# Performance work log

Hardware: AMD Instinct MI355X
Metric: run time of the kernel (lower is better)

The kernel has to match this reference:

```python
import jax, jax.numpy as jnp
import numpy as np

B, C, H, W = 4, 512, 64, 64
CK = C // 8  # key/query channels


def setup_inputs() -> dict:
    key = jax.random.key(0)
    ks = jax.random.split(key, 4)
    x = jax.random.normal(ks[0], (B, C, H, W), dtype=jnp.float32)
    # 1x1 conv weights -> plain [out, in] matrices; fan-in scaled like torch default-ish
    Wf = jax.random.normal(ks[1], (CK, C), dtype=jnp.float32) * (1.0 / np.sqrt(C))
    Wg = jax.random.normal(ks[2], (CK, C), dtype=jnp.float32) * (1.0 / np.sqrt(C))
    Wh = jax.random.normal(ks[3], (C, C), dtype=jnp.float32) * (1.0 / np.sqrt(C))
    bf = jnp.zeros((CK,), dtype=jnp.float32)
    bg = jnp.zeros((CK,), dtype=jnp.float32)
    bh = jnp.zeros((C,), dtype=jnp.float32)
    gamma = jnp.zeros((1,), dtype=jnp.float32)
    return {"x": x, "Wf": Wf, "bf": bf, "Wg": Wg, "bg": bg, "Wh": Wh, "bh": bh, "gamma": gamma}


def reference(x, Wf, bf, Wg, bg, Wh, bh, gamma):
    b, c, h, w = x.shape
    n = h * w
    xf = x.reshape(b, c, n)  # [B, C, N]
    # 1x1 convs == per-pixel linear maps
    f = jnp.einsum('kc,bcn->bkn', Wf, xf) + bf[None, :, None]  # [B, CK, N]
    g = jnp.einsum('kc,bcn->bkn', Wg, xf) + bg[None, :, None]  # [B, CK, N]
    hx = jnp.einsum('oc,bcn->bon', Wh, xf) + bh[None, :, None]  # [B, C, N]
    # energy[b,i,j] = sum_k f[b,k,i] * g[b,k,j]  (f_x.permute(0,2,1) @ g_x)
    energy = jnp.einsum('bki,bkj->bij', f, g)  # [B, N, N]
    attention = jax.nn.softmax(energy, axis=-1)
    # out[b,c,i] = sum_j hx[b,c,j] * attention[b,i,j]  (h_x @ attention^T)
    out = jnp.einsum('bcj,bij->bci', hx, attention)  # [B, C, N]
    out = out.reshape(b, c, h, w)
    return gamma[0] * out + x
```

## Files before the change

### kernel.cpp

```cpp
#include <hip/hip_runtime.h>
#include <hip/hip_bf16.h>

#define NB 4
#define CC 512
#define NN 4096
#define CKK 64

typedef _Float16 f16x4 __attribute__((ext_vector_type(4)));
typedef _Float16 f16x8 __attribute__((ext_vector_type(8)));
typedef float    f32x4 __attribute__((ext_vector_type(4)));

__device__ __forceinline__ void g2l16(const _Float16* g, _Float16* l) {
    __builtin_amdgcn_global_load_lds(
        (const __attribute__((address_space(1))) void*)g,
        (__attribute__((address_space(3))) void*)l, 16, 0, 0);
}

__device__ __forceinline__ void stage_tile(const _Float16* __restrict__ g, int ldg,
                                           _Float16* lds, int lane, int wave) {
    #pragma unroll
    for (int r = 0; r < 2; r++) {
        int q = r * 4 + wave;
        int row = q * 16 + (lane >> 2);
        int col = (lane & 3) * 8;
        g2l16(g + (size_t)row * ldg + col, lds + q * 512 + lane * 8);
    }
}

__launch_bounds__(256)
__global__ void convert_w(const float* __restrict__ Wf, const float* __restrict__ bf_,
                          const float* __restrict__ Wg, const float* __restrict__ bg_,
                          const float* __restrict__ Wh, const float* __restrict__ bh_,
                          _Float16* __restrict__ Wall, float* __restrict__ Ball) {
    int o = blockIdx.x;
    int t = threadIdx.x;
    const float* src;
    if (o < 64)       src = Wf + (size_t)o * CC;
    else if (o < 128) src = Wg + (size_t)(o - 64) * CC;
    else              src = Wh + (size_t)(o - 128) * CC;
    Wall[(size_t)o * CC + t]       = (_Float16)src[t];
    Wall[(size_t)o * CC + 256 + t] = (_Float16)src[256 + t];
    if (t == 0)
        Ball[o] = (o < 64) ? bf_[o] : (o < 128 ? bg_[o - 64] : bh_[o - 128]);
}

__launch_bounds__(256)
__global__ void proj_mfma(const float* __restrict__ x, const _Float16* __restrict__ Wall,
                          const float* __restrict__ Ball,
                          _Float16* __restrict__ Ft, _Float16* __restrict__ Gt,
                          _Float16* __restrict__ Hx) {
    const int N = NN, C = CC;
    int n0 = blockIdx.x * 128;
    int o0 = blockIdx.y * 128;
    int b  = blockIdx.z;
    const float* xb = x + (size_t)b * C * N;
    __shared__ _Float16 As[128 * 32];
    __shared__ _Float16 Bs[32 * 128];
    int tid = threadIdx.x, lane = tid & 63, wave = tid >> 6;
    int wm = wave & 1, wn = wave >> 1, lrow = lane & 15, quad = lane >> 4;
    int bk = tid >> 3;
    int bs = tid & 7;
    f32x4 acc[4][4] = {};
    for (int kc = 0; kc < C; kc += 32) {
        __syncthreads();
        stage_tile(Wall + (size_t)o0 * C + kc, C, As, lane, wave);
        const float* xr = xb + (size_t)(kc + bk) * N + n0 + bs * 16;
        float4 v0 = *(const float4*)(xr);
        float4 v1 = *(const float4*)(xr + 4);
        float4 v2 = *(const float4*)(xr + 8);
        float4 v3 = *(const float4*)(xr + 12);
        f16x8 h0 = { (_Float16)v0.x, (_Float16)v0.y, (_Float16)v0.z, (_Float16)v0.w,
                     (_Float16)v1.x, (_Float16)v1.y, (_Float16)v1.z, (_Float16)v1.w };
        f16x8 h1 = { (_Float16)v2.x, (_Float16)v2.y, (_Float16)v2.z, (_Float16)v2.w,
                     (_Float16)v3.x, (_Float16)v3.y, (_Float16)v3.z, (_Float16)v3.w };
        *(f16x8*)(Bs + bk * 128 + bs * 16)     = h0;
        *(f16x8*)(Bs + bk * 128 + bs * 16 + 8) = h1;
        __syncthreads();
        f16x8 af[4], bfr[4];
        #pragma unroll
        for (int mi = 0; mi < 4; mi++)
            af[mi] = *(const f16x8*)(As + (wm * 64 + mi * 16 + lrow) * 32 + quad * 8);
        #pragma unroll
        for (int ni = 0; ni < 4; ni++) {
            int n = wn * 64 + ni * 16 + lrow;
            #pragma unroll
            for (int j = 0; j < 8; j++)
                bfr[ni][j] = Bs[(quad * 8 + j) * 128 + n];
        }
        #pragma unroll
        for (int mi = 0; mi < 4; mi++)
            #pragma unroll
            for (int ni = 0; ni < 4; ni++)
                acc[mi][ni] = __builtin_amdgcn_mfma_f32_16x16x32_f16(af[mi], bfr[ni], acc[mi][ni], 0, 0, 0);
    }
    float bias_r[4][4];
    #pragma unroll
    for (int mi = 0; mi < 4; mi++)
        #pragma unroll
        for (int r = 0; r < 4; r++)
            bias_r[mi][r] = Ball[o0 + wm * 64 + mi * 16 + quad * 4 + r];
    _Float16* Ftb = Ft + (size_t)b * NN * CKK;
    _Float16* Gtb = Gt + (size_t)b * NN * CKK;
    _Float16* Hxb = Hx + (size_t)b * CC * N;
    #pragma unroll
    for (int mi = 0; mi < 4; mi++)
        #pragma unroll
        for (int ni = 0; ni < 4; ni++)
            #pragma unroll
            for (int r = 0; r < 4; r++) {
                int o = o0 + wm * 64 + mi * 16 + quad * 4 + r;
                int n = n0 + wn * 64 + ni * 16 + lrow;
                _Float16 v = (_Float16)(acc[mi][ni][r] + bias_r[mi][r]);
                if (o < 64)       Ftb[(size_t)n * CKK + o] = v;
                else if (o < 128) Gtb[(size_t)n * CKK + (o - 64)] = v;
                else              Hxb[(size_t)(o - 128) * N + n] = v;
            }
}

__launch_bounds__(256)
__global__ void energy_mfma(const _Float16* __restrict__ Ft, const _Float16* __restrict__ Gt,
                            _Float16* __restrict__ E, int r0, int Rstr) {
    const int N = NN;
    int b = blockIdx.z;
    const _Float16* Arow = Ft + (size_t)b * N * CKK + (size_t)(r0 + blockIdx.y * 128) * CKK;
    const _Float16* Brow = Gt + (size_t)b * N * CKK + (size_t)(blockIdx.x * 128) * CKK;
    _Float16* Eb = E + (size_t)b * Rstr * N + (size_t)blockIdx.y * 128 * N + blockIdx.x * 128;
    __shared__ _Float16 As[128 * 32];
    __shared__ _Float16 Bs[128 * 32];
    int tid = threadIdx.x, lane = tid & 63, wave = tid >> 6;
    int wm = wave & 1, wn = wave >> 1, lrow = lane & 15, quad = lane >> 4;
    f32x4 acc[4][4] = {};
    #pragma unroll
    for (int kc = 0; kc < CKK; kc += 32) {
        __syncthreads();
        stage_tile(Arow + kc, CKK, As, lane, wave);
        stage_tile(Brow + kc, CKK, Bs, lane, wave);
        __syncthreads();
        f16x8 af[4], bf[4];
        #pragma unroll
        for (int mi = 0; mi < 4; mi++)
            af[mi] = *(const f16x8*)(As + (wm * 64 + mi * 16 + lrow) * 32 + quad * 8);
        #pragma unroll
        for (int ni = 0; ni < 4; ni++)
            bf[ni] = *(const f16x8*)(Bs + (wn * 64 + ni * 16 + lrow) * 32 + quad * 8);
        #pragma unroll
        for (int mi = 0; mi < 4; mi++)
            #pragma unroll
            for (int ni = 0; ni < 4; ni++)
                acc[mi][ni] = __builtin_amdgcn_mfma_f32_16x16x32_f16(af[mi], bf[ni], acc[mi][ni], 0, 0, 0);
    }
    #pragma unroll
    for (int mi = 0; mi < 4; mi++)
        #pragma unroll
        for (int ni = 0; ni < 4; ni++)
            #pragma unroll
            for (int r = 0; r < 4; r++) {
                int il = wm * 64 + mi * 16 + quad * 4 + r;
                int j  = wn * 64 + ni * 16 + lrow;
                Eb[(size_t)il * N + j] = (_Float16)acc[mi][ni][r];
            }
}

__launch_bounds__(256)
__global__ void softmax_f16(_Float16* __restrict__ E, size_t bstride) {
    _Float16* p = E + blockIdx.y * bstride + (size_t)blockIdx.x * NN;
    int tid = threadIdx.x;
    f16x8 v0 = *(const f16x8*)(p + tid * 8);
    f16x8 v1 = *(const f16x8*)(p + 2048 + tid * 8);
    float f[16];
    #pragma unroll
    for (int j = 0; j < 8; j++) { f[j] = (float)v0[j]; f[8 + j] = (float)v1[j]; }
    float m = -1e30f;
    #pragma unroll
    for (int j = 0; j < 16; j++) m = fmaxf(m, f[j]);
    #pragma unroll
    for (int off = 32; off > 0; off >>= 1) m = fmaxf(m, __shfl_down(m, off));
    __shared__ float red[8];
    int wave = tid >> 6, lane = tid & 63;
    if (lane == 0) red[wave] = m;
    __syncthreads();
    m = fmaxf(fmaxf(red[0], red[1]), fmaxf(red[2], red[3]));
    float s = 0.f;
    #pragma unroll
    for (int j = 0; j < 16; j++) { f[j] = __expf(f[j] - m); s += f[j]; }
    #pragma unroll
    for (int off = 32; off > 0; off >>= 1) s += __shfl_down(s, off);
    if (lane == 0) red[4 + wave] = s;
    __syncthreads();
    s = red[4] + red[5] + red[6] + red[7];
    float inv = 1.0f / s;
    #pragma unroll
    for (int j = 0; j < 8; j++) { v0[j] = (_Float16)(f[j] * inv); v1[j] = (_Float16)(f[8 + j] * inv); }
    *(f16x8*)(p + tid * 8) = v0;
    *(f16x8*)(p + 2048 + tid * 8) = v1;
}

__launch_bounds__(256)
__global__ void out_mfma(const _Float16* __restrict__ Hx, const _Float16* __restrict__ P,
                         const float* __restrict__ x, const float* __restrict__ gamma,
                         float* __restrict__ out, int r0, int Rstr) {
    const int N = NN, C = CC;
    int b = blockIdx.z;
    int i0l = blockIdx.x * 128;
    int c0  = blockIdx.y * 128;
    const _Float16* Arow = Hx + (size_t)b * C * N + (size_t)c0 * N;
    const _Float16* Brow = P  + (size_t)b * Rstr * N + (size_t)i0l * N;
    __shared__ _Float16 As[128 * 32];
    __shared__ _Float16 Bs[128 * 32];
    int tid = threadIdx.x, lane = tid & 63, wave = tid >> 6;
    int wm = wave & 1, wn = wave >> 1, lrow = lane & 15, quad = lane >> 4;
    f32x4 acc[4][4] = {};
    for (int kc = 0; kc < N; kc += 32) {
        __syncthreads();
        stage_tile(Arow + kc, N, As, lane, wave);
        stage_tile(Brow + kc, N, Bs, lane, wave);
        __syncthreads();
        f16x8 af[4], bf[4];
        #pragma unroll
        for (int mi = 0; mi < 4; mi++)
            af[mi] = *(const f16x8*)(As + (wm * 64 + mi * 16 + lrow) * 32 + quad * 8);
        #pragma unroll
        for (int ni = 0; ni < 4; ni++)
            bf[ni] = *(const f16x8*)(Bs + (wn * 64 + ni * 16 + lrow) * 32 + quad * 8);
        #pragma unroll
        for (int mi = 0; mi < 4; mi++)
            #pragma unroll
            for (int ni = 0; ni < 4; ni++)
                acc[mi][ni] = __builtin_amdgcn_mfma_f32_16x16x32_f16(af[mi], bf[ni], acc[mi][ni], 0, 0, 0);
    }
    float gv = gamma[0];
    const float* xb = x + (size_t)b * C * N;
    float* ob = out + (size_t)b * C * N;
    int ig0 = r0 + i0l;
    #pragma unroll
    for (int mi = 0; mi < 4; mi++)
        #pragma unroll
        for (int ni = 0; ni < 4; ni++)
            #pragma unroll
            for (int r = 0; r < 4; r++) {
                int c = c0 + wm * 64 + mi * 16 + quad * 4 + r;
                int i = ig0 + wn * 64 + ni * 16 + lrow;
                ob[(size_t)c * N + i] = gv * acc[mi][ni][r] + xb[(size_t)c * N + i];
            }
}

extern "C" void kernel_launch(void* const* d_in, const int* in_sizes, int n_in,
                              void* d_out, int out_size, void* d_ws, size_t ws_size,
                              hipStream_t stream) {
    const float* x     = (const float*)d_in[0];
    const float* Wf    = (const float*)d_in[1];
    const float* bf    = (const float*)d_in[2];
    const float* Wg    = (const float*)d_in[3];
    const float* bg    = (const float*)d_in[4];
    const float* Wh    = (const float*)d_in[5];
    const float* bh    = (const float*)d_in[6];
    const float* gamma = (const float*)d_in[7];
    float* out = (float*)d_out;

    const int B = NB, C = CC, N = NN;

    char* wsb = (char*)d_ws;
    _Float16* Wall = (_Float16*)wsb;
    float*    Ball = (float*)(wsb + ((size_t)768 << 10));
    _Float16* Ft = (_Float16*)(wsb + ((size_t)1 << 20));
    _Float16* Gt = (_Float16*)(wsb + ((size_t)3 << 20));
    _Float16* Hx = (_Float16*)(wsb + ((size_t)5 << 20));
    _Float16* E  = (_Float16*)(wsb + ((size_t)21 << 20));
    size_t base = (size_t)21 << 20;
    size_t avail = (ws_size > base) ? ws_size - base : 0;
    size_t bytesPer128 = (size_t)B * N * 2 * 128;
    int R = (int)(avail / bytesPer128) * 128;
    if (R > N) R = N;
    if (R < 128) R = 128;

    convert_w<<<dim3(640), dim3(256), 0, stream>>>(Wf, bf, Wg, bg, Wh, bh, Wall, Ball);
    proj_mfma<<<dim3(N / 128, 5, B), dim3(256), 0, stream>>>(x, Wall, Ball, Ft, Gt, Hx);

    for (int r0 = 0; r0 < N; r0 += R) {
        int rows = (R < N - r0) ? R : (N - r0);
        energy_mfma<<<dim3(N / 128, rows / 128, B), dim3(256), 0, stream>>>(Ft, Gt, E, r0, R);
        softmax_f16<<<dim3(rows, B), dim3(256), 0, stream>>>(E, (size_t)R * N);
        out_mfma<<<dim3(rows / 128, C / 128, B), dim3(256), 0, stream>>>(Hx, E, x, gamma, out, r0, R);
    }
}
```

Baseline: 288.8 us.

## Fuse softmax statistics into energy epilogue and apply exp in output GEMM

```diff
diff --git a/kernel.cpp b/kernel.cpp
--- a/kernel.cpp
+++ b/kernel.cpp
@@ -119,7 +119,8 @@
 
 __launch_bounds__(256)
 __global__ void energy_mfma(const _Float16* __restrict__ Ft, const _Float16* __restrict__ Gt,
-                            _Float16* __restrict__ E, int r0, int Rstr) {
+                            _Float16* __restrict__ E, float* __restrict__ Mpart,
+                            float* __restrict__ Lpart, int r0, int Rstr) {
     const int N = NN;
     int b = blockIdx.z;
     const _Float16* Arow = Ft + (size_t)b * N * CKK + (size_t)(r0 + blockIdx.y * 128) * CKK;
@@ -127,6 +128,7 @@
     _Float16* Eb = E + (size_t)b * Rstr * N + (size_t)blockIdx.y * 128 * N + blockIdx.x * 128;
     __shared__ _Float16 As[128 * 32];
     __shared__ _Float16 Bs[128 * 32];
+    __shared__ float Sred[640];
     int tid = threadIdx.x, lane = tid & 63, wave = tid >> 6;
     int wm = wave & 1, wn = wave >> 1, lrow = lane & 15, quad = lane >> 4;
     f32x4 acc[4][4] = {};
@@ -159,44 +161,87 @@
                 int j  = wn * 64 + ni * 16 + lrow;
                 Eb[(size_t)il * N + j] = (_Float16)acc[mi][ni][r];
             }
-}
-
-__launch_bounds__(256)
-__global__ void softmax_f16(_Float16* __restrict__ E, size_t bstride) {
-    _Float16* p = E + blockIdx.y * bstride + (size_t)blockIdx.x * NN;
-    int tid = threadIdx.x;
-    f16x8 v0 = *(const f16x8*)(p + tid * 8);
-    f16x8 v1 = *(const f16x8*)(p + 2048 + tid * 8);
-    float f[16];
-    #pragma unroll
-    for (int j = 0; j < 8; j++) { f[j] = (float)v0[j]; f[8 + j] = (float)v1[j]; }
+    float mloc[16];
+    #pragma unroll
+    for (int mi = 0; mi < 4; mi++)
+        #pragma unroll
+        for (int r = 0; r < 4; r++) {
+            float v = acc[mi][0][r];
+            #pragma unroll
+            for (int ni = 1; ni < 4; ni++) v = fmaxf(v, acc[mi][ni][r]);
+            mloc[mi * 4 + r] = v;
+        }
+    #pragma unroll
+    for (int off = 1; off < 16; off <<= 1)
+        #pragma unroll
+        for (int s = 0; s < 16; s++)
+            mloc[s] = fmaxf(mloc[s], __shfl_xor(mloc[s], off));
+    {
+        float v = mloc[0];
+        #pragma unroll
+        for (int s = 1; s < 16; s++) v = (lrow == s) ? mloc[s] : v;
+        int row = wm * 64 + (lrow >> 2) * 16 + quad * 4 + (lrow & 3);
+        Sred[wn * 128 + row] = v;
+    }
+    __syncthreads();
+    if (tid < 128) Sred[512 + tid] = fmaxf(Sred[tid], Sred[128 + tid]);
+    __syncthreads();
+    float lloc[16];
+    #pragma unroll
+    for (int mi = 0; mi < 4; mi++)
+        #pragma unroll
+        for (int r = 0; r < 4; r++) {
+            int row = wm * 64 + mi * 16 + quad * 4 + r;
+            float m = Sred[512 + row];
+            float s = 0.f;
+            #pragma unroll
+            for (int ni = 0; ni < 4; ni++)
+                s += __expf((float)(_Float16)acc[mi][ni][r] - m);
+            lloc[mi * 4 + r] = s;
+        }
+    #pragma unroll
+    for (int off = 1; off < 16; off <<= 1)
+        #pragma unroll
+        for (int s = 0; s < 16; s++)
+            lloc[s] += __shfl_xor(lloc[s], off);
+    {
+        float v = lloc[0];
+        #pragma unroll
+        for (int s = 1; s < 16; s++) v = (lrow == s) ? lloc[s] : v;
+        int row = wm * 64 + (lrow >> 2) * 16 + quad * 4 + (lrow & 3);
+        Sred[256 + wn * 128 + row] = v;
+    }
+    __syncthreads();
+    if (tid < 128) {
+        size_t sidx = ((size_t)b * 32 + blockIdx.x) * Rstr + blockIdx.y * 128 + tid;
+        Mpart[sidx] = Sred[512 + tid];
+        Lpart[sidx] = Sred[256 + tid] + Sred[256 + 128 + tid];
+    }
+}
+
+__launch_bounds__(256)
+__global__ void combine_stats(const float* __restrict__ Mpart, const float* __restrict__ Lpart,
+                              float* __restrict__ Mrow, float* __restrict__ Linv,
+                              int rows, int Rstr) {
+    int b = blockIdx.y;
+    int i = blockIdx.x * 256 + threadIdx.x;
+    if (i >= rows) return;
+    const float* mp = Mpart + (size_t)b * 32 * Rstr + i;
+    const float* lp = Lpart + (size_t)b * 32 * Rstr + i;
     float m = -1e30f;
     #pragma unroll
-    for (int j = 0; j < 16; j++) m = fmaxf(m, f[j]);
-    #pragma unroll
-    for (int off = 32; off > 0; off >>= 1) m = fmaxf(m, __shfl_down(m, off));
-    __shared__ float red[8];
-    int wave = tid >> 6, lane = tid & 63;
-    if (lane == 0) red[wave] = m;
-    __syncthreads();
-    m = fmaxf(fmaxf(red[0], red[1]), fmaxf(red[2], red[3]));
-    float s = 0.f;
-    #pragma unroll
-    for (int j = 0; j < 16; j++) { f[j] = __expf(f[j] - m); s += f[j]; }
-    #pragma unroll
-    for (int off = 32; off > 0; off >>= 1) s += __shfl_down(s, off);
-    if (lane == 0) red[4 + wave] = s;
-    __syncthreads();
-    s = red[4] + red[5] + red[6] + red[7];
-    float inv = 1.0f / s;
-    #pragma unroll
-    for (int j = 0; j < 8; j++) { v0[j] = (_Float16)(f[j] * inv); v1[j] = (_Float16)(f[8 + j] * inv); }
-    *(f16x8*)(p + tid * 8) = v0;
-    *(f16x8*)(p + 2048 + tid * 8) = v1;
+    for (int jt = 0; jt < 32; jt++) m = fmaxf(m, mp[(size_t)jt * Rstr]);
+    float l = 0.f;
+    #pragma unroll
+    for (int jt = 0; jt < 32; jt++)
+        l += lp[(size_t)jt * Rstr] * __expf(mp[(size_t)jt * Rstr] - m);
+    Mrow[(size_t)b * Rstr + i] = m;
+    Linv[(size_t)b * Rstr + i] = 1.0f / l;
 }
 
 __launch_bounds__(256)
 __global__ void out_mfma(const _Float16* __restrict__ Hx, const _Float16* __restrict__ P,
+                         const float* __restrict__ Mrow, const float* __restrict__ Linv,
                          const float* __restrict__ x, const float* __restrict__ gamma,
                          float* __restrict__ out, int r0, int Rstr) {
     const int N = NN, C = CC;
@@ -204,16 +249,28 @@
     int i0l = blockIdx.x * 128;
     int c0  = blockIdx.y * 128;
     const _Float16* Arow = Hx + (size_t)b * C * N + (size_t)c0 * N;
-    const _Float16* Brow = P  + (size_t)b * Rstr * N + (size_t)i0l * N;
     __shared__ _Float16 As[128 * 32];
     __shared__ _Float16 Bs[128 * 32];
     int tid = threadIdx.x, lane = tid & 63, wave = tid >> 6;
     int wm = wave & 1, wn = wave >> 1, lrow = lane & 15, quad = lane >> 4;
+    int rB = tid >> 1;
+    int cs = (tid & 1) * 16;
+    const _Float16* bsrc = P + (size_t)b * Rstr * N + (size_t)(i0l + rB) * N + cs;
+    float mrow = Mrow[(size_t)b * Rstr + i0l + rB];
     f32x4 acc[4][4] = {};
     for (int kc = 0; kc < N; kc += 32) {
         __syncthreads();
         stage_tile(Arow + kc, N, As, lane, wave);
-        stage_tile(Brow + kc, N, Bs, lane, wave);
+        f16x8 e0 = *(const f16x8*)(bsrc + kc);
+        f16x8 e1 = *(const f16x8*)(bsrc + kc + 8);
+        f16x8 p0, p1;
+        #pragma unroll
+        for (int j = 0; j < 8; j++) {
+            p0[j] = (_Float16)__expf((float)e0[j] - mrow);
+            p1[j] = (_Float16)__expf((float)e1[j] - mrow);
+        }
+        *(f16x8*)(Bs + rB * 32 + cs)     = p0;
+        *(f16x8*)(Bs + rB * 32 + cs + 8) = p1;
         __syncthreads();
         f16x8 af[4], bf[4];
         #pragma unroll
@@ -229,6 +286,10 @@
                 acc[mi][ni] = __builtin_amdgcn_mfma_f32_16x16x32_f16(af[mi], bf[ni], acc[mi][ni], 0, 0, 0);
     }
     float gv = gamma[0];
+    float linv[4];
+    #pragma unroll
+    for (int ni = 0; ni < 4; ni++)
+        linv[ni] = Linv[(size_t)b * Rstr + i0l + wn * 64 + ni * 16 + lrow];
     const float* xb = x + (size_t)b * C * N;
     float* ob = out + (size_t)b * C * N;
     int ig0 = r0 + i0l;
@@ -240,7 +301,7 @@
             for (int r = 0; r < 4; r++) {
                 int c = c0 + wm * 64 + mi * 16 + quad * 4 + r;
                 int i = ig0 + wn * 64 + ni * 16 + lrow;
-                ob[(size_t)c * N + i] = gv * acc[mi][ni][r] + xb[(size_t)c * N + i];
+                ob[(size_t)c * N + i] = gv * acc[mi][ni][r] * linv[ni] + xb[(size_t)c * N + i];
             }
 }
 
@@ -265,8 +326,12 @@
     _Float16* Ft = (_Float16*)(wsb + ((size_t)1 << 20));
     _Float16* Gt = (_Float16*)(wsb + ((size_t)3 << 20));
     _Float16* Hx = (_Float16*)(wsb + ((size_t)5 << 20));
-    _Float16* E  = (_Float16*)(wsb + ((size_t)21 << 20));
-    size_t base = (size_t)21 << 20;
+    float* Mpart = (float*)(wsb + ((size_t)21 << 20));
+    float* Lpart = (float*)(wsb + ((size_t)23 << 20));
+    float* Mrow  = (float*)(wsb + ((size_t)25 << 20));
+    float* Linv  = (float*)(wsb + ((size_t)25 << 20) + ((size_t)512 << 10));
+    _Float16* E  = (_Float16*)(wsb + ((size_t)26 << 20));
+    size_t base = (size_t)26 << 20;
     size_t avail = (ws_size > base) ? ws_size - base : 0;
     size_t bytesPer128 = (size_t)B * N * 2 * 128;
     int R = (int)(avail / bytesPer128) * 128;
@@ -278,8 +343,11 @@
 
     for (int r0 = 0; r0 < N; r0 += R) {
         int rows = (R < N - r0) ? R : (N - r0);
-        energy_mfma<<<dim3(N / 128, rows / 128, B), dim3(256), 0, stream>>>(Ft, Gt, E, r0, R);
-        softmax_f16<<<dim3(rows, B), dim3(256), 0, stream>>>(E, (size_t)R * N);
-        out_mfma<<<dim3(rows / 128, C / 128, B), dim3(256), 0, stream>>>(Hx, E, x, gamma, out, r0, R);
-    }
-}
+        energy_mfma<<<dim3(N / 128, rows / 128, B), dim3(256), 0, stream>>>(
+            Ft, Gt, E, Mpart, Lpart, r0, R);
+        combine_stats<<<dim3((rows + 255) / 256, B), dim3(256), 0, stream>>>(
+            Mpart, Lpart, Mrow, Linv, rows, R);
+        out_mfma<<<dim3(rows / 128, C / 128, B), dim3(256), 0, stream>>>(
+            Hx, E, Mrow, Linv, x, gamma, out, r0, R);
+    }
+}
```

After: 329.8 us. +14.2%, slower.
